# Optimization experiments

Hardware: AMD Instinct MI355X
Metric: run time of the kernel (lower is better)

The kernel has to match this reference:

```python
import jax, jax.numpy as jnp
import numpy as np

D = 1024      # total input features
R = 32        # number of ragged regions
RMAX = 32     # max region size (padding target)
HIDDEN = [128, 128]
H1, H2 = HIDDEN
B = 8192      # batch size


def _made_masks(r, rmax, hidden):
    """TFP AutoregressiveNetwork masks (left-to-right order, 'equal' hidden degrees,
    params=2, use_bias=False), zero-padded to rmax features."""
    order = np.arange(1, r + 1)
    degs = [order]
    for u in hidden:
        mn = min(int(degs[-1].min()), r - 1)
        degs.append(np.maximum(mn, np.ceil(np.arange(1, u + 1) * (r - 1) / float(u + 1)).astype(np.int64)))
    m1 = np.zeros((rmax, hidden[0]), bool)
    m1[:r] = degs[0][:, None] <= degs[1][None, :]
    m2 = degs[1][:, None] <= degs[2][None, :]
    mout = np.zeros((hidden[-1], rmax * 2), bool)
    out_deg = np.repeat(order, 2)  # output layout is feature-major: [feat, param]
    mout[:, :2 * r] = degs[-1][:, None] < out_deg[None, :]
    return m1, m2, mout


def setup_inputs() -> dict:
    rng = np.random.default_rng(0)
    perm = rng.permutation(D)
    sizes = rng.integers(8, RMAX + 1, size=R)
    idx = np.zeros((R, RMAX), np.int64)
    valid = np.zeros((R, RMAX), bool)
    M1 = np.zeros((R, RMAX, H1), bool)
    M2 = np.zeros((R, H1, H2), bool)
    Mout = np.zeros((R, H2, RMAX * 2), bool)
    pos = 0
    for i in range(R):
        s = int(sizes[i])
        idx[i, :s] = perm[pos:pos + s]
        pos += s
        valid[i, :s] = True
        M1[i], M2[i], Mout[i] = _made_masks(s, RMAX, HIDDEN)
    key = jax.random.key(0)
    k1, k2, k3, k4 = jax.random.split(key, 4)
    inputs = jax.random.normal(k1, (B, D), jnp.float32)
    W1 = jax.random.normal(k2, (R, RMAX, H1), jnp.float32) / np.float32(np.sqrt(RMAX))
    W2 = jax.random.normal(k3, (R, H1, H2), jnp.float32) / np.float32(np.sqrt(H1))
    Wout = jax.random.normal(k4, (R, H2, RMAX * 2), jnp.float32) / np.float32(np.sqrt(H2))
    return {"inputs": inputs, "W1": W1, "W2": W2, "Wout": Wout,
            "idx": jnp.asarray(idx), "valid": jnp.asarray(valid),
            "M1": jnp.asarray(M1), "M2": jnp.asarray(M2), "Mout": jnp.asarray(Mout)}


def reference(inputs, W1, W2, Wout, idx, valid, M1, M2, Mout):
    f = inputs.dtype
    v = valid.astype(f)                              # [R, RMAX]
    xg = jnp.take(inputs, idx, axis=1) * v           # [B, R, RMAX] ragged gather (padded)
    # MADE masked MLP (relu, no bias), batched over all regions at once
    h1 = jax.nn.relu(jnp.einsum('brd,rdh->brh', xg, W1 * M1.astype(f)))
    h2 = jax.nn.relu(jnp.einsum('brh,rhk->brk', h1, W2 * M2.astype(f)))
    out = jnp.einsum('brk,rko->bro', h2, Wout * Mout.astype(f))
    out = out.reshape(out.shape[0], out.shape[1], RMAX, 2)
    shift, log_s = out[..., 0], out[..., 1]
    # MAF inverse: u = (x - shift) * exp(-log_scale); logdet = -sum(log_scale)
    u = (xg - shift) * jnp.exp(-log_s)
    elem = -0.5 * u * u - 0.5 * jnp.log(2.0 * jnp.pi) - log_s
    ll = jnp.sum(elem * v, axis=-1)                  # [B, R]
    return ll[..., None]                             # [B, R, 1] as in tf.stack of expand_dims
```

## Files before the change

### kernel.cpp

```cpp
#include <hip/hip_runtime.h>
#include <math.h>


#define RR 32
#define DD 1024
#define HH 128
#define OO 64
#define TROWS 32
#define BLOCKS_PER_R 24
#define MAXT 11

#define SHP 136
#define SXG 40
#define SSC 136

typedef _Float16 f16x8_t __attribute__((ext_vector_type(8)));
typedef float f32x4_t __attribute__((ext_vector_type(4)));
typedef unsigned short u16;
typedef unsigned int u32;

__device__ __forceinline__ u16 f16b(float x) {
    _Float16 h = (_Float16)x;
    union { _Float16 f; u16 u; } c; c.f = h; return c.u;
}
__device__ __forceinline__ f32x4_t mfma16h(f16x8_t a, f16x8_t b, f32x4_t c) {
    return __builtin_amdgcn_mfma_f32_16x16x32_f16(a, b, c, 0, 0, 0);
}

__device__ __forceinline__ void stage_block16(const float* __restrict__ W,
                                              const int* __restrict__ M,
                                              int ldc, int c0, int K, u16* dst,
                                              int tid)
{
    const int kb = tid >> 3;
    const int cb = tid & 7;
    if (kb * 4 >= K) return;
    const int k0 = kb * 4;
    float e[4][4];
#pragma unroll
    for (int i = 0; i < 4; ++i) {
        const int o = ((k0 + i) * ldc + c0 + 4 * cb) >> 2;
        float4 w = ((const float4*)W)[o];
        int4   m = ((const int4*)M)[o];
        e[i][0] = m.x ? w.x : 0.f; e[i][1] = m.y ? w.y : 0.f;
        e[i][2] = m.z ? w.z : 0.f; e[i][3] = m.w ? w.w : 0.f;
    }
#pragma unroll
    for (int j = 0; j < 4; ++j) {
        ushort4 p;
        p.x = f16b(e[0][j]); p.y = f16b(e[1][j]);
        p.z = f16b(e[2][j]); p.w = f16b(e[3][j]);
        *(ushort4*)&dst[(4 * cb + j) * SSC + k0] = p;
    }
}

__device__ __forceinline__ void relu_store16(u16* __restrict__ dst, int o, f32x4_t a)
{
    ushort4 s;
    s.x = f16b(fmaxf(a[0], 0.f));
    s.y = f16b(fmaxf(a[1], 0.f));
    s.z = f16b(fmaxf(a[2], 0.f));
    s.w = f16b(fmaxf(a[3], 0.f));
    *(ushort4*)&dst[o] = s;
}

__global__ __launch_bounds__(512, 6)
void made_flow_r16(const float* __restrict__ inputs,
                   const float* __restrict__ W1,
                   const float* __restrict__ W2,
                   const float* __restrict__ Wout,
                   const int* __restrict__ idx,
                   const int* __restrict__ valid,
                   const int* __restrict__ M1,
                   const int* __restrict__ M2,
                   const int* __restrict__ Mout,
                   float* __restrict__ out)
{
    __shared__ __align__(16) u16 h1s[2][TROWS * SHP];
    __shared__ __align__(16) u16 h2s[2][TROWS * SHP];
    __shared__ __align__(16) u16 xgh[4][TROWS * SXG];
    __shared__ __align__(16) float red_all[MAXT][TROWS][4];
    __shared__ int   idx_s[RR];
    __shared__ float v_s[RR];

    u16* const scr  = h1s[0];
    u16* const scr2 = h1s[1];

    const int tid  = threadIdx.x;
    const int r    = blockIdx.x / BLOCKS_PER_R;
    const int rb   = blockIdx.x % BLOCKS_PER_R;
    const int ts   = (rb < 16) ? 11 * rb : 176 + 10 * (rb - 16);
    const int nt   = (rb < 16) ? 11 : 10;

    const int lane = tid & 63;
    const int wave = tid >> 6;
    const int q    = lane >> 4;
    const int l16  = lane & 15;
    const int wm3  = wave & 3;
    const int ni3  = wave >> 2;

    if (tid < RR) {
        idx_s[tid] = idx[r * RR + tid];
        v_s[tid]   = valid[r * RR + tid] ? 1.f : 0.f;
    }

    f16x8_t a1;
    f16x8_t a2[4];
    f16x8_t ao[4];
    {
        const float* W1r = W1 + r * RR * HH;   const int* M1r = M1 + r * RR * HH;
        const float* W2r = W2 + r * HH * HH;   const int* M2r = M2 + r * HH * HH;
        const float* Wor = Wout + r * HH * OO; const int* Mor = Mout + r * HH * OO;
        const int c = wave >> 1, h = wave & 1;
        for (int i = 0; i < 2; ++i) {
            __syncthreads();
            if (tid < 256) stage_block16(W2r, M2r, HH, 32 * (2 * i),     HH, scr,  tid);
            else           stage_block16(W2r, M2r, HH, 32 * (2 * i + 1), HH, scr2, tid - 256);
            __syncthreads();
            if (c == 2 * i) {
#pragma unroll
                for (int ks = 0; ks < 4; ++ks)
                    a2[ks] = *(const f16x8_t*)&scr[(16 * h + l16) * SSC + ks * 32 + q * 8];
            } else if (c == 2 * i + 1) {
#pragma unroll
                for (int ks = 0; ks < 4; ++ks)
                    a2[ks] = *(const f16x8_t*)&scr2[(16 * h + l16) * SSC + ks * 32 + q * 8];
            }
        }
        {
            __syncthreads();
            if (tid < 256) stage_block16(Wor, Mor, OO, 0,  HH, scr,  tid);
            else           stage_block16(Wor, Mor, OO, 32, HH, scr2, tid - 256);
            __syncthreads();
            const u16* s = (wm3 >> 1) ? scr2 : scr;
#pragma unroll
            for (int ks = 0; ks < 4; ++ks)
                ao[ks] = *(const f16x8_t*)&s[(16 * (wm3 & 1) + l16) * SSC + ks * 32 + q * 8];
        }
        for (int i = 0; i < 2; ++i) {
            __syncthreads();
            if (tid < 256) stage_block16(W1r, M1r, HH, 32 * (2 * i),     RR, scr,  tid);
            else           stage_block16(W1r, M1r, HH, 32 * (2 * i + 1), RR, scr2, tid - 256);
            __syncthreads();
            if (c == 2 * i)          a1 = *(const f16x8_t*)&scr [(16 * h + l16) * SSC + q * 8];
            else if (c == 2 * i + 1) a1 = *(const f16x8_t*)&scr2[(16 * h + l16) * SSC + q * 8];
        }
    }
    __syncthreads();

    const f32x4_t zero4 = {0.f, 0.f, 0.f, 0.f};
    const int grow = tid >> 4;
    const int gg   = tid & 15;

    const int   ci0 = idx_s[2 * gg], ci1 = idx_s[2 * gg + 1];
    const float cv0 = v_s[2 * gg],   cv1 = v_s[2 * gg + 1];
    const int   gbase = (ts * TROWS + grow) * DD;

    {
        float a0 = inputs[gbase + ci0] * cv0;
        float a1v = inputs[gbase + ci1] * cv1;
        float b0 = inputs[gbase + TROWS * DD + ci0] * cv0;
        float b1 = inputs[gbase + TROWS * DD + ci1] * cv1;
        *(u32*)&xgh[0][grow * SXG + 2 * gg] = (u32)f16b(a0) | ((u32)f16b(a1v) << 16);
        *(u32*)&xgh[1][grow * SXG + 2 * gg] = (u32)f16b(b0) | ((u32)f16b(b1) << 16);
    }
    __syncthreads();

    {
#pragma unroll
        for (int ni = 0; ni < 2; ++ni) {
            f16x8_t b = *(const f16x8_t*)&xgh[0][(16 * ni + l16) * SXG + q * 8];
            f32x4_t a = mfma16h(a1, b, zero4);
            relu_store16(h1s[0], (16 * ni + l16) * SHP + 16 * wave + 4 * q, a);
        }
    }

    for (int t = 0; t <= nt; ++t) {
        __syncthreads();

        const bool doP2  = (t < nt);
        const bool doP3  = (t >= 1);
        const bool doP1n = (t + 1 < nt);
        const bool doG   = (t + 2 < nt);

        float gx0, gx1;
        if (doG) {
            const int base = gbase + (t + 2) * (TROWS * DD);
            gx0 = inputs[base + ci0] * cv0;
            gx1 = inputs[base + ci1] * cv1;
        }

        f32x4_t acc3 = zero4;
        if (doP3) {
            const u16* h2b = h2s[(t - 1) & 1];
#pragma unroll
            for (int ks = 0; ks < 4; ++ks) {
                f16x8_t b = *(const f16x8_t*)&h2b[(16 * ni3 + l16) * SHP + ks * 32 + q * 8];
                acc3 = mfma16h(ao[ks], b, acc3);
            }
        }

        if (doP2) {
            const u16* h1b = h1s[t & 1];
            u16*       h2b = h2s[t & 1];
            f32x4_t acc[2] = {zero4, zero4};
#pragma unroll
            for (int ks = 0; ks < 4; ++ks) {
#pragma unroll
                for (int ni = 0; ni < 2; ++ni) {
                    f16x8_t b = *(const f16x8_t*)&h1b[(16 * ni + l16) * SHP + ks * 32 + q * 8];
                    acc[ni] = mfma16h(a2[ks], b, acc[ni]);
                }
            }
#pragma unroll
            for (int ni = 0; ni < 2; ++ni)
                relu_store16(h2b, (16 * ni + l16) * SHP + 16 * wave + 4 * q, acc[ni]);
        }

        if (doP1n) {
            const u16* xb  = xgh[(t + 1) & 3];
            u16*       h1b = h1s[(t + 1) & 1];
#pragma unroll
            for (int ni = 0; ni < 2; ++ni) {
                f16x8_t b = *(const f16x8_t*)&xb[(16 * ni + l16) * SXG + q * 8];
                f32x4_t a = mfma16h(a1, b, zero4);
                relu_store16(h1b, (16 * ni + l16) * SHP + 16 * wave + 4 * q, a);
            }
        }

        if (doP3) {
            const int j0 = 8 * wm3 + 2 * q;
            const float vj0 = v_s[j0], vj1 = v_s[j0 + 1];
            const int row = 16 * ni3 + l16;
            u32 xw = *(const u32*)&xgh[(t - 1) & 3][row * SXG + j0];
            union { u32 u; _Float16 h[2]; } xc; xc.u = xw;
            const float xv0 = (float)xc.h[0], xv1 = (float)xc.h[1];
            const float u0 = (xv0 - acc3[0]) * __expf(-acc3[1]);
            const float u1 = (xv1 - acc3[2]) * __expf(-acc3[3]);
            float p = (-0.5f * u0 * u0 - 0.91893853320467266954f - acc3[1]) * vj0
                    + (-0.5f * u1 * u1 - 0.91893853320467266954f - acc3[3]) * vj1;
            p += __shfl_xor(p, 16, 64);
            p += __shfl_xor(p, 32, 64);
            if (q == 0) red_all[t - 1][row][wm3] = p;
        }

        if (doG) {
            *(u32*)&xgh[(t + 2) & 3][grow * SXG + 2 * gg] =
                (u32)f16b(gx0) | ((u32)f16b(gx1) << 16);
        }
    }

    __syncthreads();
    if (tid < nt * TROWS) {
        const int tt  = tid >> 5;
        const int row = tid & 31;
        float4 rv = *(const float4*)&red_all[tt][row][0];
        out[((ts + tt) * TROWS + row) * RR + r] =
            rv.x + rv.y + rv.z + rv.w;
    }
}

extern "C" void kernel_launch(void* const* d_in, const int* in_sizes, int n_in,
                              void* d_out, int out_size, void* d_ws, size_t ws_size,
                              hipStream_t stream)
{
    const float* inputs = (const float*)d_in[0];
    const float* W1     = (const float*)d_in[1];
    const float* W2     = (const float*)d_in[2];
    const float* Wout   = (const float*)d_in[3];
    const int*   idx    = (const int*)d_in[4];
    const int*   valid  = (const int*)d_in[5];
    const int*   M1     = (const int*)d_in[6];
    const int*   M2     = (const int*)d_in[7];
    const int*   Mout   = (const int*)d_in[8];
    float*       out    = (float*)d_out;

    hipLaunchKernelGGL(made_flow_r16, dim3(RR * BLOCKS_PER_R), dim3(512), 0, stream,
                       inputs, W1, W2, Wout, idx, valid, M1, M2, Mout, out);
}
```

Before: 120.4 us.

## Specialize waves per MLP stage instead of splitting every stage across all waves

Work is now divided by stage rather than spread evenly. Waves 0-3 each compute a 32x32 tile of layer 2, waves 4-5 compute the output layer plus the log-likelihood epilogue, and waves 6-7 compute layer 1 for the next tile, with each wave holding 8 weight fragments in registers. The aim is to cut redundant B-operand LDS reads, since each loaded fragment now feeds two MFMAs, and to cut divergent per-stage branching in every wave. The per-wave load is uneven (layer 2 needs 16 MFMAs, output 16 plus the epilogue, layer 1 8), so the slowest wave group may set the per-step critical path, and register pressure rises.

```diff
diff --git a/kernel.cpp b/kernel.cpp
--- a/kernel.cpp
+++ b/kernel.cpp
@@ -65,7 +65,7 @@
 }
 
 __global__ __launch_bounds__(512, 6)
-void made_flow_r16(const float* __restrict__ inputs,
+void made_flow_r18(const float* __restrict__ inputs,
                    const float* __restrict__ W1,
                    const float* __restrict__ W2,
                    const float* __restrict__ Wout,
@@ -96,35 +96,36 @@
     const int wave = tid >> 6;
     const int q    = lane >> 4;
     const int l16  = lane & 15;
-    const int wm3  = wave & 3;
-    const int ni3  = wave >> 2;
+    const int w2   = wave - 4;
+    const int w1r  = wave - 6;
 
     if (tid < RR) {
         idx_s[tid] = idx[r * RR + tid];
         v_s[tid]   = valid[r * RR + tid] ? 1.f : 0.f;
     }
 
-    f16x8_t a1;
-    f16x8_t a2[4];
-    f16x8_t ao[4];
+    f16x8_t wf[8];
     {
         const float* W1r = W1 + r * RR * HH;   const int* M1r = M1 + r * RR * HH;
         const float* W2r = W2 + r * HH * HH;   const int* M2r = M2 + r * HH * HH;
         const float* Wor = Wout + r * HH * OO; const int* Mor = Mout + r * HH * OO;
-        const int c = wave >> 1, h = wave & 1;
         for (int i = 0; i < 2; ++i) {
             __syncthreads();
             if (tid < 256) stage_block16(W2r, M2r, HH, 32 * (2 * i),     HH, scr,  tid);
             else           stage_block16(W2r, M2r, HH, 32 * (2 * i + 1), HH, scr2, tid - 256);
             __syncthreads();
-            if (c == 2 * i) {
+            if (wave == 2 * i) {
 #pragma unroll
                 for (int ks = 0; ks < 4; ++ks)
-                    a2[ks] = *(const f16x8_t*)&scr[(16 * h + l16) * SSC + ks * 32 + q * 8];
-            } else if (c == 2 * i + 1) {
+#pragma unroll
+                    for (int mi = 0; mi < 2; ++mi)
+                        wf[2 * ks + mi] = *(const f16x8_t*)&scr[(16 * mi + l16) * SSC + ks * 32 + q * 8];
+            } else if (wave == 2 * i + 1) {
 #pragma unroll
                 for (int ks = 0; ks < 4; ++ks)
-                    a2[ks] = *(const f16x8_t*)&scr2[(16 * h + l16) * SSC + ks * 32 + q * 8];
+#pragma unroll
+                    for (int mi = 0; mi < 2; ++mi)
+                        wf[2 * ks + mi] = *(const f16x8_t*)&scr2[(16 * mi + l16) * SSC + ks * 32 + q * 8];
             }
         }
         {
@@ -132,57 +133,77 @@
             if (tid < 256) stage_block16(Wor, Mor, OO, 0,  HH, scr,  tid);
             else           stage_block16(Wor, Mor, OO, 32, HH, scr2, tid - 256);
             __syncthreads();
-            const u16* s = (wm3 >> 1) ? scr2 : scr;
-#pragma unroll
-            for (int ks = 0; ks < 4; ++ks)
-                ao[ks] = *(const f16x8_t*)&s[(16 * (wm3 & 1) + l16) * SSC + ks * 32 + q * 8];
+            if (wave == 4) {
+#pragma unroll
+                for (int ks = 0; ks < 4; ++ks)
+#pragma unroll
+                    for (int mi = 0; mi < 2; ++mi)
+                        wf[2 * ks + mi] = *(const f16x8_t*)&scr[(16 * mi + l16) * SSC + ks * 32 + q * 8];
+            } else if (wave == 5) {
+#pragma unroll
+                for (int ks = 0; ks < 4; ++ks)
+#pragma unroll
+                    for (int mi = 0; mi < 2; ++mi)
+                        wf[2 * ks + mi] = *(const f16x8_t*)&scr2[(16 * mi + l16) * SSC + ks * 32 + q * 8];
+            }
         }
         for (int i = 0; i < 2; ++i) {
             __syncthreads();
             if (tid < 256) stage_block16(W1r, M1r, HH, 32 * (2 * i),     RR, scr,  tid);
             else           stage_block16(W1r, M1r, HH, 32 * (2 * i + 1), RR, scr2, tid - 256);
             __syncthreads();
-            if (c == 2 * i)          a1 = *(const f16x8_t*)&scr [(16 * h + l16) * SSC + q * 8];
-            else if (c == 2 * i + 1) a1 = *(const f16x8_t*)&scr2[(16 * h + l16) * SSC + q * 8];
+            if (wave == 6 + i) {
+#pragma unroll
+                for (int mi = 0; mi < 2; ++mi) {
+                    wf[mi]     = *(const f16x8_t*)&scr [(16 * mi + l16) * SSC + q * 8];
+                    wf[2 + mi] = *(const f16x8_t*)&scr2[(16 * mi + l16) * SSC + q * 8];
+                }
+            }
         }
     }
     __syncthreads();
+
+    const int ew2 = (w2 < 0 || w2 > 1) ? 0 : w2;
+    float vjm[2][2];
+#pragma unroll
+    for (int mi = 0; mi < 2; ++mi) {
+        vjm[mi][0] = v_s[16 * ew2 + 8 * mi + 2 * q];
+        vjm[mi][1] = v_s[16 * ew2 + 8 * mi + 2 * q + 1];
+    }
 
     const f32x4_t zero4 = {0.f, 0.f, 0.f, 0.f};
     const int grow = tid >> 4;
     const int gg   = tid & 15;
-
     const int   ci0 = idx_s[2 * gg], ci1 = idx_s[2 * gg + 1];
     const float cv0 = v_s[2 * gg],   cv1 = v_s[2 * gg + 1];
     const int   gbase = (ts * TROWS + grow) * DD;
 
     {
-        float a0 = inputs[gbase + ci0] * cv0;
+        float a0  = inputs[gbase + ci0] * cv0;
         float a1v = inputs[gbase + ci1] * cv1;
-        float b0 = inputs[gbase + TROWS * DD + ci0] * cv0;
-        float b1 = inputs[gbase + TROWS * DD + ci1] * cv1;
+        float b0  = inputs[gbase + TROWS * DD + ci0] * cv0;
+        float b1  = inputs[gbase + TROWS * DD + ci1] * cv1;
         *(u32*)&xgh[0][grow * SXG + 2 * gg] = (u32)f16b(a0) | ((u32)f16b(a1v) << 16);
         *(u32*)&xgh[1][grow * SXG + 2 * gg] = (u32)f16b(b0) | ((u32)f16b(b1) << 16);
     }
     __syncthreads();
 
-    {
+    if (wave >= 6) {
 #pragma unroll
         for (int ni = 0; ni < 2; ++ni) {
             f16x8_t b = *(const f16x8_t*)&xgh[0][(16 * ni + l16) * SXG + q * 8];
-            f32x4_t a = mfma16h(a1, b, zero4);
-            relu_store16(h1s[0], (16 * ni + l16) * SHP + 16 * wave + 4 * q, a);
+#pragma unroll
+            for (int mi = 0; mi < 4; ++mi) {
+                f32x4_t a = mfma16h(wf[mi], b, zero4);
+                relu_store16(h1s[0], (16 * ni + l16) * SHP + 64 * w1r + 16 * mi + 4 * q, a);
+            }
         }
     }
 
     for (int t = 0; t <= nt; ++t) {
         __syncthreads();
 
-        const bool doP2  = (t < nt);
-        const bool doP3  = (t >= 1);
-        const bool doP1n = (t + 1 < nt);
-        const bool doG   = (t + 2 < nt);
-
+        const bool doG = (t + 2 < nt);
         float gx0, gx1;
         if (doG) {
             const int base = gbase + (t + 2) * (TROWS * DD);
@@ -190,58 +211,76 @@
             gx1 = inputs[base + ci1] * cv1;
         }
 
-        f32x4_t acc3 = zero4;
-        if (doP3) {
-            const u16* h2b = h2s[(t - 1) & 1];
-#pragma unroll
-            for (int ks = 0; ks < 4; ++ks) {
-                f16x8_t b = *(const f16x8_t*)&h2b[(16 * ni3 + l16) * SHP + ks * 32 + q * 8];
-                acc3 = mfma16h(ao[ks], b, acc3);
-            }
-        }
-
-        if (doP2) {
-            const u16* h1b = h1s[t & 1];
-            u16*       h2b = h2s[t & 1];
-            f32x4_t acc[2] = {zero4, zero4};
-#pragma unroll
-            for (int ks = 0; ks < 4; ++ks) {
+        if (wave < 4) {
+            if (t < nt) {
+                const u16* h1b = h1s[t & 1];
+                u16*       h2b = h2s[t & 1];
+                f32x4_t acc[2][2] = {{zero4, zero4}, {zero4, zero4}};
+#pragma unroll
+                for (int ks = 0; ks < 4; ++ks) {
+#pragma unroll
+                    for (int ni = 0; ni < 2; ++ni) {
+                        f16x8_t b = *(const f16x8_t*)&h1b[(16 * ni + l16) * SHP + ks * 32 + q * 8];
+#pragma unroll
+                        for (int mi = 0; mi < 2; ++mi)
+                            acc[mi][ni] = mfma16h(wf[2 * ks + mi], b, acc[mi][ni]);
+                    }
+                }
+#pragma unroll
+                for (int mi = 0; mi < 2; ++mi)
+#pragma unroll
+                    for (int ni = 0; ni < 2; ++ni)
+                        relu_store16(h2b, (16 * ni + l16) * SHP + 32 * wave + 16 * mi + 4 * q,
+                                     acc[mi][ni]);
+            }
+        } else if (wave < 6) {
+            if (t >= 1) {
+                const u16* h2b = h2s[(t - 1) & 1];
+                f32x4_t a3[2][2] = {{zero4, zero4}, {zero4, zero4}};
+#pragma unroll
+                for (int ks = 0; ks < 4; ++ks) {
+#pragma unroll
+                    for (int ni = 0; ni < 2; ++ni) {
+                        f16x8_t b = *(const f16x8_t*)&h2b[(16 * ni + l16) * SHP + ks * 32 + q * 8];
+#pragma unroll
+                        for (int mi = 0; mi < 2; ++mi)
+                            a3[mi][ni] = mfma16h(wf[2 * ks + mi], b, a3[mi][ni]);
+                    }
+                }
+#pragma unroll
+                for (int mi = 0; mi < 2; ++mi) {
+                    const int j0 = 16 * ew2 + 8 * mi + 2 * q;
+#pragma unroll
+                    for (int ni = 0; ni < 2; ++ni) {
+                        const int row = 16 * ni + l16;
+                        u32 xw = *(const u32*)&xgh[(t - 1) & 3][row * SXG + j0];
+                        union { u32 u; _Float16 h[2]; } xc; xc.u = xw;
+                        const float xv0 = (float)xc.h[0], xv1 = (float)xc.h[1];
+                        f32x4_t a = a3[mi][ni];
+                        const float u0 = (xv0 - a[0]) * __expf(-a[1]);
+                        const float u1 = (xv1 - a[2]) * __expf(-a[3]);
+                        float p = (-0.5f * u0 * u0 - 0.91893853320467266954f - a[1]) * vjm[mi][0]
+                                + (-0.5f * u1 * u1 - 0.91893853320467266954f - a[3]) * vjm[mi][1];
+                        p += __shfl_xor(p, 16, 64);
+                        p += __shfl_xor(p, 32, 64);
+                        if (q == 0) red_all[t - 1][row][2 * ew2 + mi] = p;
+                    }
+                }
+            }
+        } else {
+            if (t + 1 < nt) {
+                const u16* xb  = xgh[(t + 1) & 3];
+                u16*       h1b = h1s[(t + 1) & 1];
 #pragma unroll
                 for (int ni = 0; ni < 2; ++ni) {
-                    f16x8_t b = *(const f16x8_t*)&h1b[(16 * ni + l16) * SHP + ks * 32 + q * 8];
-                    acc[ni] = mfma16h(a2[ks], b, acc[ni]);
-                }
-            }
-#pragma unroll
-            for (int ni = 0; ni < 2; ++ni)
-                relu_store16(h2b, (16 * ni + l16) * SHP + 16 * wave + 4 * q, acc[ni]);
-        }
-
-        if (doP1n) {
-            const u16* xb  = xgh[(t + 1) & 3];
-            u16*       h1b = h1s[(t + 1) & 1];
-#pragma unroll
-            for (int ni = 0; ni < 2; ++ni) {
-                f16x8_t b = *(const f16x8_t*)&xb[(16 * ni + l16) * SXG + q * 8];
-                f32x4_t a = mfma16h(a1, b, zero4);
-                relu_store16(h1b, (16 * ni + l16) * SHP + 16 * wave + 4 * q, a);
-            }
-        }
-
-        if (doP3) {
-            const int j0 = 8 * wm3 + 2 * q;
-            const float vj0 = v_s[j0], vj1 = v_s[j0 + 1];
-            const int row = 16 * ni3 + l16;
-            u32 xw = *(const u32*)&xgh[(t - 1) & 3][row * SXG + j0];
-            union { u32 u; _Float16 h[2]; } xc; xc.u = xw;
-            const float xv0 = (float)xc.h[0], xv1 = (float)xc.h[1];
-            const float u0 = (xv0 - acc3[0]) * __expf(-acc3[1]);
-            const float u1 = (xv1 - acc3[2]) * __expf(-acc3[3]);
-            float p = (-0.5f * u0 * u0 - 0.91893853320467266954f - acc3[1]) * vj0
-                    + (-0.5f * u1 * u1 - 0.91893853320467266954f - acc3[3]) * vj1;
-            p += __shfl_xor(p, 16, 64);
-            p += __shfl_xor(p, 32, 64);
-            if (q == 0) red_all[t - 1][row][wm3] = p;
+                    f16x8_t b = *(const f16x8_t*)&xb[(16 * ni + l16) * SXG + q * 8];
+#pragma unroll
+                    for (int mi = 0; mi < 4; ++mi) {
+                        f32x4_t a = mfma16h(wf[mi], b, zero4);
+                        relu_store16(h1b, (16 * ni + l16) * SHP + 64 * w1r + 16 * mi + 4 * q, a);
+                    }
+                }
+            }
         }
 
         if (doG) {
@@ -275,6 +314,6 @@
     const int*   Mout   = (const int*)d_in[8];
     float*       out    = (float*)d_out;
 
-    hipLaunchKernelGGL(made_flow_r16, dim3(RR * BLOCKS_PER_R), dim3(512), 0, stream,
+    hipLaunchKernelGGL(made_flow_r18, dim3(RR * BLOCKS_PER_R), dim3(512), 0, stream,
                        inputs, W1, W2, Wout, idx, valid, M1, M2, Mout, out);
 }
```

Result: slower. 141.6 us (+17.6%).
